# Optimization experiments

Measured on AMD Instinct MI355X. Metric: run time of the kernel, lower is better.

Reference implementation:

```python
import jax, jax.numpy as jnp
import numpy as np

B, IN, OUT = 65536, 1024, 1024
NB, D, H, L = 16, 32, 64, 4      # n_bundles, bundle_dim, norm_mlp hidden, n_latent_layers
TOT = NB * D                      # total latent dim = 512 (also encoder/decoder hidden)


def setup_inputs() -> dict:
    key = jax.random.key(0)
    ks = jax.random.split(key, 20)
    rn = lambda k, shape, s=0.02: (jax.random.normal(k, shape, dtype=jnp.float32) * s)
    return {
        "x": jax.random.normal(ks[0], (B, IN), dtype=jnp.float32),
        # encoder: Linear(IN,TOT), Linear(TOT,TOT), Linear(TOT,TOT)
        "enc_w1": rn(ks[1], (TOT, IN)), "enc_b1": jnp.zeros((TOT,), jnp.float32),
        "enc_w2": rn(ks[2], (TOT, TOT)), "enc_b2": jnp.zeros((TOT,), jnp.float32),
        "enc_w3": rn(ks[3], (TOT, TOT)), "enc_b3": jnp.zeros((TOT,), jnp.float32),
        # per-latent-layer norm_mlp: Linear(NB,H)+b, Linear(H,H)+b, Linear(H,NB) no bias
        "mlp1_w": rn(ks[4], (L, H, NB)), "mlp1_b": jnp.zeros((L, H), jnp.float32),
        "mlp2_w": rn(ks[5], (L, H, H)),  "mlp2_b": jnp.zeros((L, H), jnp.float32),
        "mlp3_w": rn(ks[6], (L, NB, H)),
        # mixing_weights[i][j] has shape (d_i, d_j); homogeneous -> [L,NB,NB,D,D], init 0.01*randn
        "mix_w": rn(ks[7], (L, NB, NB, D, D), 0.01),
        "gate_bias": jnp.zeros((L, NB), jnp.float32),
        # decoder: Linear(TOT,TOT), Linear(TOT,TOT), Linear(TOT,OUT)
        "dec_w1": rn(ks[8], (TOT, TOT)), "dec_b1": jnp.zeros((TOT,), jnp.float32),
        "dec_w2": rn(ks[9], (TOT, TOT)), "dec_b2": jnp.zeros((TOT,), jnp.float32),
        "dec_w3": rn(ks[10], (OUT, TOT)), "dec_b3": jnp.zeros((OUT,), jnp.float32),
    }


def _gelu(v):
    return jax.nn.gelu(v, approximate=False)  # torch nn.GELU default (erf)


def _soft_equivariant(z, m1w, m1b, m2w, m2b, m3w, mw, gb):
    # z: [B, TOT] -> bundles [B, NB, D] (homogeneous dims, contiguous split == reshape)
    zb = z.reshape(z.shape[0], NB, D)
    norms = jnp.linalg.norm(zb, axis=-1) + 1e-8          # [B, NB]
    h = _gelu(norms @ m1w.T + m1b)                        # [B, H]
    h = _gelu(h @ m2w.T + m2b)                            # [B, H]
    scales = jax.nn.softplus(h @ m3w.T)                   # [B, NB]
    equi = zb * scales[:, :, None]                        # [B, NB, D]
    # mixed_i = sum_j F.linear(bundles[j], W[i][j]) = bundles[j] @ W[i][j].T
    mixed = jnp.einsum('bjd,ijed->bie', zb, mw)           # [B, NB, D]
    gates = jax.nn.sigmoid(gb)                            # [NB]
    combined = equi + gates[None, :, None] * mixed        # [B, NB, D]
    return z + combined.reshape(z.shape[0], TOT)          # residual


def reference(x, enc_w1, enc_b1, enc_w2, enc_b2, enc_w3, enc_b3,
              mlp1_w, mlp1_b, mlp2_w, mlp2_b, mlp3_w, mix_w, gate_bias,
              dec_w1, dec_b1, dec_w2, dec_b2, dec_w3, dec_b3):
    # encoder
    z = _gelu(x @ enc_w1.T + enc_b1)
    z = _gelu(z @ enc_w2.T + enc_b2)
    z = z @ enc_w3.T + enc_b3
    # latent dynamics: L SoftEquivariantLayers (fixed small loop over layers)
    for l in range(L):
        z = _soft_equivariant(z, mlp1_w[l], mlp1_b[l], mlp2_w[l], mlp2_b[l],
                              mlp3_w[l], mix_w[l], gate_bias[l])
    # decoder
    y = _gelu(z @ dec_w1.T + dec_b1)
    y = _gelu(y @ dec_w2.T + dec_b2)
    return y @ dec_w3.T + dec_b3
```

## Files before the change

### kernel.cpp

```cpp
#include <hip/hip_runtime.h>
#include <hip/hip_bf16.h>

typedef float f32x4 __attribute__((ext_vector_type(4)));
typedef __bf16 bf16x8 __attribute__((ext_vector_type(8)));
typedef unsigned short u16x8 __attribute__((ext_vector_type(8)));
typedef unsigned short u16;

#define SMEM_BYTES 155904
#define ZA_OFF 0
#define ZB_OFF 65536
#define NRM_OFF 131072
#define H_OFF 135168
#define SCL_OFF 151808

__device__ __forceinline__ u16 f2bf(float f) {
  unsigned int u = __float_as_uint(f);
  u += 0x7FFFu + ((u >> 16) & 1u);
  return (u16)(u >> 16);
}
__device__ __forceinline__ float bf2f(u16 s) {
  return __uint_as_float(((unsigned int)s) << 16);
}
__device__ __forceinline__ float gelu_f(float x) {
  return 0.5f * x * (1.0f + erff(x * 0.70710678118654752f));
}
__device__ __forceinline__ bf16x8 ldg_bf16x8(const u16* p) {
  return *(const bf16x8*)p;
}

__global__ void cvt_all(const float* __restrict__ e1, const float* __restrict__ e2,
                        const float* __restrict__ e3, const float* __restrict__ d1,
                        const float* __restrict__ d2, const float* __restrict__ d3,
                        const float* __restrict__ mx, u16* __restrict__ dst)
{
  int i = blockIdx.x * blockDim.x + threadIdx.x;
  int stride = gridDim.x * blockDim.x;
  for (; i < 3145728; i += stride) {
    float v;
    if (i < 524288)        v = e1[i];
    else if (i < 786432)   v = e2[i - 524288];
    else if (i < 1048576)  v = e3[i - 786432];
    else if (i < 1310720)  v = d1[i - 1048576];
    else if (i < 1572864)  v = d2[i - 1310720];
    else if (i < 2097152)  v = d3[i - 1572864];
    else {
      int j = i - 2097152;
      int l = j >> 18, rem = j & 262143;
      int o = rem >> 9, k = rem & 511;
      int bi = o >> 5, e = o & 31, jj = k >> 5, dd = k & 31;
      v = mx[(((l * 16 + bi) * 16 + jj) * 32 + e) * 32 + dd];
    }
    dst[i] = f2bf(v);
  }
}

template<int EPI>
__device__ __forceinline__ void gemm512(char* __restrict__ smem, int inOff, int outOff,
    const u16* __restrict__ W, const float* __restrict__ bias,
    const float* __restrict__ gateBias, float* __restrict__ outG, int nOff, int m0)
{
  __syncthreads();
  const int tid = threadIdx.x;
  const int lane = tid & 63;
  const int wid = tid >> 6;
  const int c0 = wid << 6;
  const int r16 = lane & 15;
  const int kg = (lane >> 4) << 3;
  const int sw = (r16 & 7) << 4;
  const char* zin = smem + inOff;

  f32x4 acc[4][4] = {};
  #pragma unroll 4
  for (int ks = 0; ks < 16; ++ks) {
    const int kk = ks << 5;
    bf16x8 av[4], bv[4];
    #pragma unroll
    for (int nt = 0; nt < 4; ++nt)
      bv[nt] = ldg_bf16x8(W + (size_t)(nOff + c0 + nt * 16 + r16) * 512 + kk + kg);
    #pragma unroll
    for (int mt = 0; mt < 4; ++mt)
      av[mt] = *(const bf16x8*)(zin + (mt * 16 + r16) * 1024 + (((kk + kg) << 1) ^ sw));
    #pragma unroll
    for (int mt = 0; mt < 4; ++mt)
      #pragma unroll
      for (int nt = 0; nt < 4; ++nt)
        acc[mt][nt] = __builtin_amdgcn_mfma_f32_16x16x32_bf16(av[mt], bv[nt], acc[mt][nt], 0, 0, 0);
  }

  const float* scl = (const float*)(smem + SCL_OFF);
  char* zout = smem + outOff;
  #pragma unroll
  for (int nt = 0; nt < 4; ++nt) {
    const int col = c0 + nt * 16 + r16;
    float bv_ = 0.f, gate = 0.f;
    if constexpr (EPI == 0 || EPI == 1 || EPI == 3) bv_ = bias[nOff + col];
    if constexpr (EPI == 2) gate = 1.f / (1.f + expf(-gateBias[col >> 5]));
    #pragma unroll
    for (int mt = 0; mt < 4; ++mt) {
      #pragma unroll
      for (int r = 0; r < 4; ++r) {
        const int row = mt * 16 + ((lane >> 4) << 2) + r;
        const int zb = row * 1024 + ((col << 1) ^ ((row & 7) << 4));
        float v = acc[mt][nt][r];
        if constexpr (EPI == 0) {
          *(u16*)(zout + zb) = f2bf(gelu_f(v + bv_));
        } else if constexpr (EPI == 1) {
          *(u16*)(zout + zb) = f2bf(v + bv_);
        } else if constexpr (EPI == 2) {
          float sc = scl[row * 16 + (col >> 5)];
          float zo = bf2f(*(const u16*)(zin + zb));
          *(u16*)(zout + zb) = f2bf(zo * (1.f + sc) + gate * v);
        } else {
          outG[(size_t)(m0 + row) * 1024 + nOff + col] = v + bv_;
        }
      }
    }
  }
}

__device__ __forceinline__ void norm_phase(char* __restrict__ smem, int zOff,
    const float* __restrict__ w1, const float* __restrict__ b1,
    const float* __restrict__ w2, const float* __restrict__ b2,
    const float* __restrict__ w3)
{
  __syncthreads();
  const int tid = threadIdx.x;
  float* nrm = (float*)(smem + NRM_OFF);
  float* h   = (float*)(smem + H_OFF);
  float* scl = (float*)(smem + SCL_OFF);
  const char* z = smem + zOff;

  #pragma unroll
  for (int p = 0; p < 2; ++p) {
    int task = tid + p * 512;
    int r = task >> 4, b = task & 15;
    float ss = 0.f;
    #pragma unroll
    for (int s = 0; s < 4; ++s) {
      u16x8 v = *(const u16x8*)(z + r * 1024 + ((b * 64 + s * 16) ^ ((r & 7) << 4)));
      #pragma unroll
      for (int j = 0; j < 8; ++j) { float f = bf2f(v[j]); ss += f * f; }
    }
    nrm[r * 16 + b] = sqrtf(ss) + 1e-8f;
  }
  __syncthreads();

  const int j = tid & 63;
  const int r0w = tid >> 6;
  {
    float a[8];
    #pragma unroll
    for (int p = 0; p < 8; ++p) a[p] = b1[j];
    #pragma unroll
    for (int i = 0; i < 16; ++i) {
      float wv = w1[j * 16 + i];
      #pragma unroll
      for (int p = 0; p < 8; ++p) a[p] += nrm[(r0w + 8 * p) * 16 + i] * wv;
    }
    #pragma unroll
    for (int p = 0; p < 8; ++p) h[(r0w + 8 * p) * 65 + j] = gelu_f(a[p]);
  }
  __syncthreads();
  {
    float a[8];
    #pragma unroll
    for (int p = 0; p < 8; ++p) a[p] = b2[j];
    for (int k = 0; k < 64; ++k) {
      float wv = w2[j * 64 + k];
      #pragma unroll
      for (int p = 0; p < 8; ++p) a[p] += h[(r0w + 8 * p) * 65 + k] * wv;
    }
    __syncthreads();
    #pragma unroll
    for (int p = 0; p < 8; ++p) h[(r0w + 8 * p) * 65 + j] = gelu_f(a[p]);
  }
  __syncthreads();
  {
    const int b = tid & 15;
    const int r0 = tid >> 4;
    float a0 = 0.f, a1 = 0.f;
    for (int k = 0; k < 64; ++k) {
      float wv = w3[b * 64 + k];
      a0 += h[r0 * 65 + k] * wv;
      a1 += h[(r0 + 32) * 65 + k] * wv;
    }
    a0 = (a0 > 20.f) ? a0 : log1pf(expf(a0));
    a1 = (a1 > 20.f) ? a1 : log1pf(expf(a1));
    scl[r0 * 16 + b] = a0;
    scl[(r0 + 32) * 16 + b] = a1;
  }
  __syncthreads();
}

__global__ __launch_bounds__(512, 2)
void ugn_mega(const float* __restrict__ x,
              const float* __restrict__ enc_b1, const float* __restrict__ enc_b2,
              const float* __restrict__ enc_b3,
              const float* __restrict__ mlp1_w, const float* __restrict__ mlp1_b,
              const float* __restrict__ mlp2_w, const float* __restrict__ mlp2_b,
              const float* __restrict__ mlp3_w, const float* __restrict__ gate_b,
              const float* __restrict__ dec_b1, const float* __restrict__ dec_b2,
              const float* __restrict__ dec_b3,
              const u16* __restrict__ wE1, const u16* __restrict__ wE2,
              const u16* __restrict__ wE3, const u16* __restrict__ wMix,
              const u16* __restrict__ wD1, const u16* __restrict__ wD2,
              const u16* __restrict__ wD3, float* __restrict__ out)
{
  extern __shared__ char smem[];
  const int m0 = blockIdx.x << 6;
  const int tid = threadIdx.x;
  const int lane = tid & 63;
  const int wid = tid >> 6;
  const int c0 = wid << 6;
  const int r16 = lane & 15;
  const int kg = (lane >> 4) << 3;
  const int swz = (r16 & 7) << 4;

  {
    char* stage = smem + NRM_OFF;
    const float* xs = x + (size_t)m0 * 1024;
    const int xr = tid >> 3;
    const int kp = (tid & 7) << 3;
    float4 v0 = *(const float4*)(xs + (size_t)xr * 1024 + kp);
    float4 v1 = *(const float4*)(xs + (size_t)xr * 1024 + kp + 4);
    f32x4 acc[4][4] = {};
    for (int c = 0; c < 16; ++c) {
      u16x8 u;
      u[0] = f2bf(v0.x); u[1] = f2bf(v0.y); u[2] = f2bf(v0.z); u[3] = f2bf(v0.w);
      u[4] = f2bf(v1.x); u[5] = f2bf(v1.y); u[6] = f2bf(v1.z); u[7] = f2bf(v1.w);
      *(u16x8*)(stage + xr * 128 + ((kp << 1) ^ ((xr & 7) << 4))) = u;
      __syncthreads();
      if (c < 15) {
        const float* src = xs + (size_t)xr * 1024 + (c + 1) * 64 + kp;
        v0 = *(const float4*)src;
        v1 = *(const float4*)(src + 4);
      }
      #pragma unroll
      for (int ks = 0; ks < 2; ++ks) {
        const int kk = ks << 5;
        bf16x8 av[4], bv[4];
        #pragma unroll
        for (int nt = 0; nt < 4; ++nt)
          bv[nt] = ldg_bf16x8(wE1 + (size_t)(c0 + nt * 16 + r16) * 1024 + c * 64 + kk + kg);
        #pragma unroll
        for (int mt = 0; mt < 4; ++mt)
          av[mt] = *(const bf16x8*)(stage + (mt * 16 + r16) * 128 + (((kk + kg) << 1) ^ swz));
        #pragma unroll
        for (int mt = 0; mt < 4; ++mt)
          #pragma unroll
          for (int nt = 0; nt < 4; ++nt)
            acc[mt][nt] = __builtin_amdgcn_mfma_f32_16x16x32_bf16(av[mt], bv[nt], acc[mt][nt], 0, 0, 0);
      }
      __syncthreads();
    }
    char* zout = smem + ZA_OFF;
    #pragma unroll
    for (int nt = 0; nt < 4; ++nt) {
      const int col = c0 + nt * 16 + r16;
      const float bb = enc_b1[col];
      #pragma unroll
      for (int mt = 0; mt < 4; ++mt) {
        #pragma unroll
        for (int r = 0; r < 4; ++r) {
          const int row = mt * 16 + ((lane >> 4) << 2) + r;
          *(u16*)(zout + row * 1024 + ((col << 1) ^ ((row & 7) << 4))) =
              f2bf(gelu_f(acc[mt][nt][r] + bb));
        }
      }
    }
  }

  gemm512<0>(smem, ZA_OFF, ZB_OFF, wE2, enc_b2, nullptr, nullptr, 0, m0);
  gemm512<1>(smem, ZB_OFF, ZA_OFF, wE3, enc_b3, nullptr, nullptr, 0, m0);

  #pragma unroll
  for (int l = 0; l < 4; ++l) {
    const int zi = (l & 1) ? ZB_OFF : ZA_OFF;
    const int zo = (l & 1) ? ZA_OFF : ZB_OFF;
    norm_phase(smem, zi, mlp1_w + l * 1024, mlp1_b + l * 64,
               mlp2_w + l * 4096, mlp2_b + l * 64, mlp3_w + l * 1024);
    gemm512<2>(smem, zi, zo, wMix + (size_t)l * 262144, nullptr, gate_b + l * 16,
               nullptr, 0, m0);
  }

  gemm512<0>(smem, ZA_OFF, ZB_OFF, wD1, dec_b1, nullptr, nullptr, 0, m0);
  gemm512<0>(smem, ZB_OFF, ZA_OFF, wD2, dec_b2, nullptr, nullptr, 0, m0);
  gemm512<3>(smem, ZA_OFF, ZB_OFF, wD3, dec_b3, nullptr, out, 0, m0);
  gemm512<3>(smem, ZA_OFF, ZB_OFF, wD3, dec_b3, nullptr, out, 512, m0);
}

extern "C" void kernel_launch(void* const* d_in, const int* in_sizes, int n_in,
                              void* d_out, int out_size, void* d_ws, size_t ws_size,
                              hipStream_t stream)
{
  (void)in_sizes; (void)n_in; (void)out_size; (void)ws_size;
  const float* x      = (const float*)d_in[0];
  const float* enc_w1 = (const float*)d_in[1];
  const float* enc_b1 = (const float*)d_in[2];
  const float* enc_w2 = (const float*)d_in[3];
  const float* enc_b2 = (const float*)d_in[4];
  const float* enc_w3 = (const float*)d_in[5];
  const float* enc_b3 = (const float*)d_in[6];
  const float* mlp1_w = (const float*)d_in[7];
  const float* mlp1_b = (const float*)d_in[8];
  const float* mlp2_w = (const float*)d_in[9];
  const float* mlp2_b = (const float*)d_in[10];
  const float* mlp3_w = (const float*)d_in[11];
  const float* mix_w  = (const float*)d_in[12];
  const float* gate_b = (const float*)d_in[13];
  const float* dec_w1 = (const float*)d_in[14];
  const float* dec_b1 = (const float*)d_in[15];
  const float* dec_w2 = (const float*)d_in[16];
  const float* dec_b2 = (const float*)d_in[17];
  const float* dec_w3 = (const float*)d_in[18];
  const float* dec_b3 = (const float*)d_in[19];

  u16* wBase = (u16*)d_ws;
  u16* wE1 = wBase;
  u16* wE2 = wE1 + 524288;
  u16* wE3 = wE2 + 262144;
  u16* wD1 = wE3 + 262144;
  u16* wD2 = wD1 + 262144;
  u16* wD3 = wD2 + 262144;
  u16* wMix = wD3 + 524288;

  cvt_all<<<512, 256, 0, stream>>>(enc_w1, enc_w2, enc_w3, dec_w1, dec_w2, dec_w3,
                                   mix_w, wBase);

  static int smemSet = 0;
  if (!smemSet) {
    hipFuncSetAttribute(reinterpret_cast<const void*>(&ugn_mega),
                        hipFuncAttributeMaxDynamicSharedMemorySize, SMEM_BYTES);
    smemSet = 1;
  }

  ugn_mega<<<1024, 512, SMEM_BYTES, stream>>>(
      x, enc_b1, enc_b2, enc_b3, mlp1_w, mlp1_b, mlp2_w, mlp2_b, mlp3_w, gate_b,
      dec_b1, dec_b2, dec_b3, wE1, wE2, wE3, wMix, wD1, wD2, wD3, (float*)d_out);
}
```

Before: 1.473 ms.

## Shrink row tile to 32 with in-place single LDS buffer and wider warp N-tiles

Each block now handles 32 rows with 256 threads instead of 64 rows with 512. Each wave computes a 32x128 tile (2x8 MFMA tiles) instead of 64x64. The ping-pong activation buffers are merged into one in-place buffer, guarded by an extra barrier before the epilogue. This cuts shared memory from about 156KB to 45KB so more blocks can be resident per CU. It also moves the sigmoid gate computation into the norm phase, uses wave-shuffle reductions for the bundle norms, adds s_setprio around the MFMA bursts, and uses the native bf16 conversion. The trade-off is that weight rows are reread from global/L2 twice as often per output row, and the extra synchronisation adds cost.

```diff
diff --git a/kernel.cpp b/kernel.cpp
--- a/kernel.cpp
+++ b/kernel.cpp
@@ -6,26 +6,22 @@
 typedef unsigned short u16x8 __attribute__((ext_vector_type(8)));
 typedef unsigned short u16;
 
-#define SMEM_BYTES 155904
-#define ZA_OFF 0
-#define ZB_OFF 65536
-#define NRM_OFF 131072
-#define H_OFF 135168
-#define SCL_OFF 151808
+#define SMEM_BYTES 45248
+#define Z_OFF 0
+#define NRM_OFF 32768
+#define H_OFF 34816
+#define SCL_OFF 43136
+#define GATE_OFF 45184
 
 __device__ __forceinline__ u16 f2bf(float f) {
-  unsigned int u = __float_as_uint(f);
-  u += 0x7FFFu + ((u >> 16) & 1u);
-  return (u16)(u >> 16);
+  __bf16 h = (__bf16)f;
+  return __builtin_bit_cast(u16, h);
 }
 __device__ __forceinline__ float bf2f(u16 s) {
   return __uint_as_float(((unsigned int)s) << 16);
 }
 __device__ __forceinline__ float gelu_f(float x) {
   return 0.5f * x * (1.0f + erff(x * 0.70710678118654752f));
-}
-__device__ __forceinline__ bf16x8 ldg_bf16x8(const u16* p) {
-  return *(const bf16x8*)p;
 }
 
 __global__ void cvt_all(const float* __restrict__ e1, const float* __restrict__ e2,
@@ -55,124 +51,141 @@
 }
 
 template<int EPI>
-__device__ __forceinline__ void gemm512(char* __restrict__ smem, int inOff, int outOff,
+__device__ __forceinline__ void gemm512(char* __restrict__ smem,
     const u16* __restrict__ W, const float* __restrict__ bias,
-    const float* __restrict__ gateBias, float* __restrict__ outG, int nOff, int m0)
+    float* __restrict__ outG, int nOff, int m0)
 {
   __syncthreads();
   const int tid = threadIdx.x;
   const int lane = tid & 63;
   const int wid = tid >> 6;
-  const int c0 = wid << 6;
+  const int c0 = wid << 7;
   const int r16 = lane & 15;
   const int kg = (lane >> 4) << 3;
   const int sw = (r16 & 7) << 4;
-  const char* zin = smem + inOff;
-
-  f32x4 acc[4][4] = {};
-  #pragma unroll 4
+  char* z = smem + Z_OFF;
+
+  const u16* wrow[8];
+  #pragma unroll
+  for (int nt = 0; nt < 8; ++nt)
+    wrow[nt] = W + (size_t)(nOff + c0 + nt * 16 + r16) * 512 + kg;
+  const char* arow[2];
+  #pragma unroll
+  for (int mt = 0; mt < 2; ++mt)
+    arow[mt] = z + (mt * 16 + r16) * 1024;
+
+  f32x4 acc[2][8] = {};
+  #pragma unroll 2
   for (int ks = 0; ks < 16; ++ks) {
-    const int kk = ks << 5;
-    bf16x8 av[4], bv[4];
-    #pragma unroll
-    for (int nt = 0; nt < 4; ++nt)
-      bv[nt] = ldg_bf16x8(W + (size_t)(nOff + c0 + nt * 16 + r16) * 512 + kk + kg);
-    #pragma unroll
-    for (int mt = 0; mt < 4; ++mt)
-      av[mt] = *(const bf16x8*)(zin + (mt * 16 + r16) * 1024 + (((kk + kg) << 1) ^ sw));
-    #pragma unroll
-    for (int mt = 0; mt < 4; ++mt)
-      #pragma unroll
-      for (int nt = 0; nt < 4; ++nt)
+    const int kb = (ks << 6) | (kg << 1);
+    bf16x8 av[2], bv[8];
+    #pragma unroll
+    for (int nt = 0; nt < 8; ++nt)
+      bv[nt] = *(const bf16x8*)(wrow[nt] + (ks << 5));
+    #pragma unroll
+    for (int mt = 0; mt < 2; ++mt)
+      av[mt] = *(const bf16x8*)(arow[mt] + (kb ^ sw));
+    __builtin_amdgcn_s_setprio(1);
+    #pragma unroll
+    for (int mt = 0; mt < 2; ++mt)
+      #pragma unroll
+      for (int nt = 0; nt < 8; ++nt)
         acc[mt][nt] = __builtin_amdgcn_mfma_f32_16x16x32_bf16(av[mt], bv[nt], acc[mt][nt], 0, 0, 0);
-  }
+    __builtin_amdgcn_s_setprio(0);
+  }
+
+  __syncthreads();
 
   const float* scl = (const float*)(smem + SCL_OFF);
-  char* zout = smem + outOff;
+  const float* gateL = (const float*)(smem + GATE_OFF);
   #pragma unroll
-  for (int nt = 0; nt < 4; ++nt) {
+  for (int nt = 0; nt < 8; ++nt) {
     const int col = c0 + nt * 16 + r16;
     float bv_ = 0.f, gate = 0.f;
     if constexpr (EPI == 0 || EPI == 1 || EPI == 3) bv_ = bias[nOff + col];
-    if constexpr (EPI == 2) gate = 1.f / (1.f + expf(-gateBias[col >> 5]));
-    #pragma unroll
-    for (int mt = 0; mt < 4; ++mt) {
+    if constexpr (EPI == 2) gate = gateL[col >> 5];
+    #pragma unroll
+    for (int mt = 0; mt < 2; ++mt) {
       #pragma unroll
       for (int r = 0; r < 4; ++r) {
         const int row = mt * 16 + ((lane >> 4) << 2) + r;
-        const int zb = row * 1024 + ((col << 1) ^ ((row & 7) << 4));
         float v = acc[mt][nt][r];
-        if constexpr (EPI == 0) {
-          *(u16*)(zout + zb) = f2bf(gelu_f(v + bv_));
-        } else if constexpr (EPI == 1) {
-          *(u16*)(zout + zb) = f2bf(v + bv_);
-        } else if constexpr (EPI == 2) {
-          float sc = scl[row * 16 + (col >> 5)];
-          float zo = bf2f(*(const u16*)(zin + zb));
-          *(u16*)(zout + zb) = f2bf(zo * (1.f + sc) + gate * v);
+        if constexpr (EPI == 3) {
+          outG[(size_t)(m0 + row) * 1024 + nOff + col] = v + bv_;
         } else {
-          outG[(size_t)(m0 + row) * 1024 + nOff + col] = v + bv_;
+          char* zp = z + row * 1024 + ((col << 1) ^ ((row & 7) << 4));
+          if constexpr (EPI == 0)      *(u16*)zp = f2bf(gelu_f(v + bv_));
+          else if constexpr (EPI == 1) *(u16*)zp = f2bf(v + bv_);
+          else {
+            float sc = scl[row * 16 + (col >> 5)];
+            float zo = bf2f(*(const u16*)zp);
+            *(u16*)zp = f2bf(zo * (1.f + sc) + gate * v);
+          }
         }
       }
     }
   }
 }
 
-__device__ __forceinline__ void norm_phase(char* __restrict__ smem, int zOff,
+__device__ __forceinline__ void norm_phase(char* __restrict__ smem,
     const float* __restrict__ w1, const float* __restrict__ b1,
     const float* __restrict__ w2, const float* __restrict__ b2,
-    const float* __restrict__ w3)
+    const float* __restrict__ w3, const float* __restrict__ gb)
 {
   __syncthreads();
   const int tid = threadIdx.x;
+  const int lane = tid & 63;
+  const int wv = tid >> 6;
   float* nrm = (float*)(smem + NRM_OFF);
   float* h   = (float*)(smem + H_OFF);
   float* scl = (float*)(smem + SCL_OFF);
-  const char* z = smem + zOff;
+  float* gateL = (float*)(smem + GATE_OFF);
+  const char* z = smem + Z_OFF;
 
   #pragma unroll
-  for (int p = 0; p < 2; ++p) {
-    int task = tid + p * 512;
-    int r = task >> 4, b = task & 15;
+  for (int p = 0; p < 8; ++p) {
+    const int row = p * 4 + wv;
+    u16x8 v = *(const u16x8*)(z + row * 1024 + ((lane << 4) ^ ((row & 7) << 4)));
     float ss = 0.f;
     #pragma unroll
-    for (int s = 0; s < 4; ++s) {
-      u16x8 v = *(const u16x8*)(z + r * 1024 + ((b * 64 + s * 16) ^ ((r & 7) << 4)));
-      #pragma unroll
-      for (int j = 0; j < 8; ++j) { float f = bf2f(v[j]); ss += f * f; }
-    }
-    nrm[r * 16 + b] = sqrtf(ss) + 1e-8f;
-  }
-  __syncthreads();
-
-  const int j = tid & 63;
-  const int r0w = tid >> 6;
+    for (int j = 0; j < 8; ++j) { float f = bf2f(v[j]); ss += f * f; }
+    ss += __shfl_xor(ss, 1);
+    ss += __shfl_xor(ss, 2);
+    if ((lane & 3) == 0) {
+      const int bundle = (lane >> 2) ^ ((row >> 2) & 1);
+      nrm[row * 16 + bundle] = sqrtf(ss) + 1e-8f;
+    }
+  }
+  if (tid < 16) gateL[tid] = 1.f / (1.f + expf(-gb[tid]));
+  __syncthreads();
+
   {
+    const int j = lane;
     float a[8];
     #pragma unroll
     for (int p = 0; p < 8; ++p) a[p] = b1[j];
     #pragma unroll
     for (int i = 0; i < 16; ++i) {
-      float wv = w1[j * 16 + i];
-      #pragma unroll
-      for (int p = 0; p < 8; ++p) a[p] += nrm[(r0w + 8 * p) * 16 + i] * wv;
-    }
-    #pragma unroll
-    for (int p = 0; p < 8; ++p) h[(r0w + 8 * p) * 65 + j] = gelu_f(a[p]);
+      float w = w1[j * 16 + i];
+      #pragma unroll
+      for (int p = 0; p < 8; ++p) a[p] += nrm[(wv * 8 + p) * 16 + i] * w;
+    }
+    #pragma unroll
+    for (int p = 0; p < 8; ++p) h[(wv * 8 + p) * 65 + j] = gelu_f(a[p]);
   }
   __syncthreads();
   {
+    const int j = lane;
     float a[8];
     #pragma unroll
     for (int p = 0; p < 8; ++p) a[p] = b2[j];
     for (int k = 0; k < 64; ++k) {
-      float wv = w2[j * 64 + k];
-      #pragma unroll
-      for (int p = 0; p < 8; ++p) a[p] += h[(r0w + 8 * p) * 65 + k] * wv;
-    }
-    __syncthreads();
-    #pragma unroll
-    for (int p = 0; p < 8; ++p) h[(r0w + 8 * p) * 65 + j] = gelu_f(a[p]);
+      float w = w2[j * 64 + k];
+      #pragma unroll
+      for (int p = 0; p < 8; ++p) a[p] += h[(wv * 8 + p) * 65 + k] * w;
+    }
+    #pragma unroll
+    for (int p = 0; p < 8; ++p) h[(wv * 8 + p) * 65 + j] = gelu_f(a[p]);
   }
   __syncthreads();
   {
@@ -180,19 +193,19 @@
     const int r0 = tid >> 4;
     float a0 = 0.f, a1 = 0.f;
     for (int k = 0; k < 64; ++k) {
-      float wv = w3[b * 64 + k];
-      a0 += h[r0 * 65 + k] * wv;
-      a1 += h[(r0 + 32) * 65 + k] * wv;
+      float w = w3[b * 64 + k];
+      a0 += h[r0 * 65 + k] * w;
+      a1 += h[(r0 + 16) * 65 + k] * w;
     }
     a0 = (a0 > 20.f) ? a0 : log1pf(expf(a0));
     a1 = (a1 > 20.f) ? a1 : log1pf(expf(a1));
     scl[r0 * 16 + b] = a0;
-    scl[(r0 + 32) * 16 + b] = a1;
-  }
-  __syncthreads();
-}
-
-__global__ __launch_bounds__(512, 2)
+    scl[(r0 + 16) * 16 + b] = a1;
+  }
+  __syncthreads();
+}
+
+__global__ __launch_bounds__(256, 2)
 void ugn_mega(const float* __restrict__ x,
               const float* __restrict__ enc_b1, const float* __restrict__ enc_b2,
               const float* __restrict__ enc_b3,
@@ -207,23 +220,29 @@
               const u16* __restrict__ wD3, float* __restrict__ out)
 {
   extern __shared__ char smem[];
-  const int m0 = blockIdx.x << 6;
+  const int m0 = blockIdx.x << 5;
   const int tid = threadIdx.x;
   const int lane = tid & 63;
   const int wid = tid >> 6;
-  const int c0 = wid << 6;
+  const int c0 = wid << 7;
   const int r16 = lane & 15;
   const int kg = (lane >> 4) << 3;
-  const int swz = (r16 & 7) << 4;
+  const int sw = (r16 & 7) << 4;
 
   {
     char* stage = smem + NRM_OFF;
+    char* z = smem + Z_OFF;
     const float* xs = x + (size_t)m0 * 1024;
     const int xr = tid >> 3;
     const int kp = (tid & 7) << 3;
+    const u16* wrow[8];
+    #pragma unroll
+    for (int nt = 0; nt < 8; ++nt)
+      wrow[nt] = wE1 + (size_t)(c0 + nt * 16 + r16) * 1024 + kg;
+
     float4 v0 = *(const float4*)(xs + (size_t)xr * 1024 + kp);
     float4 v1 = *(const float4*)(xs + (size_t)xr * 1024 + kp + 4);
-    f32x4 acc[4][4] = {};
+    f32x4 acc[2][8] = {};
     for (int c = 0; c < 16; ++c) {
       u16x8 u;
       u[0] = f2bf(v0.x); u[1] = f2bf(v0.y); u[2] = f2bf(v0.z); u[3] = f2bf(v0.w);
@@ -237,56 +256,54 @@
       }
       #pragma unroll
       for (int ks = 0; ks < 2; ++ks) {
-        const int kk = ks << 5;
-        bf16x8 av[4], bv[4];
+        bf16x8 av[2], bv[8];
         #pragma unroll
-        for (int nt = 0; nt < 4; ++nt)
-          bv[nt] = ldg_bf16x8(wE1 + (size_t)(c0 + nt * 16 + r16) * 1024 + c * 64 + kk + kg);
+        for (int nt = 0; nt < 8; ++nt)
+          bv[nt] = *(const bf16x8*)(wrow[nt] + c * 64 + ks * 32);
         #pragma unroll
-        for (int mt = 0; mt < 4; ++mt)
-          av[mt] = *(const bf16x8*)(stage + (mt * 16 + r16) * 128 + (((kk + kg) << 1) ^ swz));
+        for (int mt = 0; mt < 2; ++mt)
+          av[mt] = *(const bf16x8*)(stage + (mt * 16 + r16) * 128 + (((ks << 6) | (kg << 1)) ^ sw));
+        __builtin_amdgcn_s_setprio(1);
         #pragma unroll
-        for (int mt = 0; mt < 4; ++mt)
+        for (int mt = 0; mt < 2; ++mt)
           #pragma unroll
-          for (int nt = 0; nt < 4; ++nt)
+          for (int nt = 0; nt < 8; ++nt)
             acc[mt][nt] = __builtin_amdgcn_mfma_f32_16x16x32_bf16(av[mt], bv[nt], acc[mt][nt], 0, 0, 0);
+        __builtin_amdgcn_s_setprio(0);
       }
       __syncthreads();
     }
-    char* zout = smem + ZA_OFF;
-    #pragma unroll
-    for (int nt = 0; nt < 4; ++nt) {
+    #pragma unroll
+    for (int nt = 0; nt < 8; ++nt) {
       const int col = c0 + nt * 16 + r16;
       const float bb = enc_b1[col];
       #pragma unroll
-      for (int mt = 0; mt < 4; ++mt) {
+      for (int mt = 0; mt < 2; ++mt) {
         #pragma unroll
         for (int r = 0; r < 4; ++r) {
           const int row = mt * 16 + ((lane >> 4) << 2) + r;
-          *(u16*)(zout + row * 1024 + ((col << 1) ^ ((row & 7) << 4))) =
+          *(u16*)(z + row * 1024 + ((col << 1) ^ ((row & 7) << 4))) =
               f2bf(gelu_f(acc[mt][nt][r] + bb));
         }
       }
     }
   }
 
-  gemm512<0>(smem, ZA_OFF, ZB_OFF, wE2, enc_b2, nullptr, nullptr, 0, m0);
-  gemm512<1>(smem, ZB_OFF, ZA_OFF, wE3, enc_b3, nullptr, nullptr, 0, m0);
-
-  #pragma unroll
+  gemm512<0>(smem, wE2, enc_b2, nullptr, 0, m0);
+  gemm512<1>(smem, wE3, enc_b3, nullptr, 0, m0);
+
+  #pragma unroll 1
   for (int l = 0; l < 4; ++l) {
-    const int zi = (l & 1) ? ZB_OFF : ZA_OFF;
-    const int zo = (l & 1) ? ZA_OFF : ZB_OFF;
-    norm_phase(smem, zi, mlp1_w + l * 1024, mlp1_b + l * 64,
-               mlp2_w + l * 4096, mlp2_b + l * 64, mlp3_w + l * 1024);
-    gemm512<2>(smem, zi, zo, wMix + (size_t)l * 262144, nullptr, gate_b + l * 16,
-               nullptr, 0, m0);
-  }
-
-  gemm512<0>(smem, ZA_OFF, ZB_OFF, wD1, dec_b1, nullptr, nullptr, 0, m0);
-  gemm512<0>(smem, ZB_OFF, ZA_OFF, wD2, dec_b2, nullptr, nullptr, 0, m0);
-  gemm512<3>(smem, ZA_OFF, ZB_OFF, wD3, dec_b3, nullptr, out, 0, m0);
-  gemm512<3>(smem, ZA_OFF, ZB_OFF, wD3, dec_b3, nullptr, out, 512, m0);
+    norm_phase(smem, mlp1_w + l * 1024, mlp1_b + l * 64,
+               mlp2_w + l * 4096, mlp2_b + l * 64,
+               mlp3_w + l * 1024, gate_b + l * 16);
+    gemm512<2>(smem, wMix + (size_t)l * 262144, nullptr, nullptr, 0, m0);
+  }
+
+  gemm512<0>(smem, wD1, dec_b1, nullptr, 0, m0);
+  gemm512<0>(smem, wD2, dec_b2, nullptr, 0, m0);
+  gemm512<3>(smem, wD3, dec_b3, out, 0, m0);
+  gemm512<3>(smem, wD3, dec_b3, out, 512, m0);
 }
 
 extern "C" void kernel_launch(void* const* d_in, const int* in_sizes, int n_in,
@@ -334,7 +351,7 @@
     smemSet = 1;
   }
 
-  ugn_mega<<<1024, 512, SMEM_BYTES, stream>>>(
+  ugn_mega<<<2048, 256, SMEM_BYTES, stream>>>(
       x, enc_b1, enc_b2, enc_b3, mlp1_w, mlp1_b, mlp2_w, mlp2_b, mlp3_w, gate_b,
       dec_b1, dec_b2, dec_b3, wE1, wE2, wE3, wMix, wD1, wD2, wD3, (float*)d_out);
 }
```

Result: slower. 1.809 ms (+22.9%).
